# Kernel tuning notes

Hardware: AMD Instinct MI355X
Metric: run time of the kernel (lower is better)

Reference implementation:

```python
import jax, jax.numpy as jnp
import numpy as np

N_NODES = 100000
N_EDGES = 1600000
D_IN = 128
D_OUT = 128


def setup_inputs() -> dict:
    key = jax.random.key(0)
    ks = jax.random.split(key, 7)
    x = jax.random.normal(ks[0], (N_NODES, D_IN), dtype=jnp.float32)
    y = jax.random.normal(ks[1], (N_NODES, D_OUT), dtype=jnp.float32)
    edge_src = jax.random.randint(ks[2], (N_EDGES,), 0, N_NODES, dtype=jnp.int32)
    edge_dst = jax.random.randint(ks[3], (N_EDGES,), 0, N_NODES, dtype=jnp.int32)
    adj_vals = jax.random.uniform(ks[4], (N_EDGES,), dtype=jnp.float32)
    weight = jax.random.normal(ks[5], (D_IN, D_OUT), dtype=jnp.float32) * (1.0 / np.sqrt(D_IN))
    bias = jax.random.normal(ks[6], (D_OUT,), dtype=jnp.float32) * 0.01
    return {"x": x, "y": y, "edge_src": edge_src, "edge_dst": edge_dst,
            "adj_vals": adj_vals, "weight": weight, "bias": bias}


def reference(x, y, edge_src, edge_dst, adj_vals, weight, bias):
    # GraphConvolution: support = x @ W ; out = spmm(adj, support) + bias
    support = x @ weight                      # [N, d_out]
    msgs = support[edge_src] * adj_vals[:, None]   # [E, d_out] gather + scale
    agg = jax.ops.segment_sum(msgs, edge_dst, num_segments=N_NODES)  # [N, d_out]
    gc_out = agg + bias
    # ResGCN epilogue: relu(gc_out + y); dropout is identity in eval (p=0.0)
    return jax.nn.relu(gc_out + y)
```

## Files before the change

kernel.cpp:

```cpp
#include <hip/hip_runtime.h>

#define D 128
#define CE 8192
#define NB_MAX 1024
#define MAXC 512
#define EBUF 3072
#define CHUNK 1024
#define WTP 136


typedef __attribute__((ext_vector_type(8))) short bf16x8;
typedef __attribute__((ext_vector_type(4))) float f32x4;

__device__ __forceinline__ unsigned short f2bf(float f) {
  unsigned u = __float_as_uint(f);
  unsigned r = (u + 0x7fffu + ((u >> 16) & 1u)) >> 16;
  return (unsigned short)r;
}

__device__ __forceinline__ int wave_iscan(int v) {
  const int lane = threadIdx.x & 63;
#pragma unroll
  for (int off = 1; off < 64; off <<= 1) {
    int u = __shfl_up(v, off, 64);
    if (lane >= off) v += u;
  }
  return v;
}

__device__ __forceinline__ int seg_find(const int* pref, int nC, int i) {
  int lo = 0, hi = nC;
  while (hi - lo > 1) {
    int mid = (lo + hi) >> 1;
    if (pref[mid] <= i) lo = mid; else hi = mid;
  }
  return lo;
}

__global__ __launch_bounds__(256) void convert_kernel(
    const float4* __restrict__ x4, ushort4* __restrict__ xb4, int n4, int nxblk,
    const float* __restrict__ w, unsigned short* __restrict__ wt) {
  int bid = blockIdx.x;
  if (bid < nxblk) {
    int i = bid * 256 + threadIdx.x;
    if (i < n4) {
      float4 v = x4[i];
      ushort4 r;
      r.x = f2bf(v.x);
      r.y = f2bf(v.y);
      r.z = f2bf(v.z);
      r.w = f2bf(v.w);
      xb4[i] = r;
    }
  } else {
    int idx = (bid - nxblk) * 256 + threadIdx.x;
    int n = idx >> 7, k = idx & 127;
    wt[n * WTP + k] = f2bf(w[k * D + n]);
  }
}

__global__ __launch_bounds__(1024) void chunk_sort_kernel(
    const int* __restrict__ src, const int* __restrict__ dst,
    const float* __restrict__ adj, int2* __restrict__ edges,
    unsigned short* __restrict__ ofs, int nE, int nB) {
  __shared__ int2 stage[CE];
  __shared__ int h[NB_MAX + 4];
  __shared__ int wsum[16];
  const int t = threadIdx.x;
  const int c = blockIdx.x;
  const int e0 = c * CE;
  const int n = min(CE, nE - e0);
  const int lane = t & 63, wid = t >> 6;

  for (int i = t; i < NB_MAX + 4; i += 1024) h[i] = 0;
  __syncthreads();

  int dreg[8];
#pragma unroll
  for (int k = 0; k < 8; ++k) {
    int i = k * 1024 + t;
    if (i < n) {
      int d = dst[e0 + i];
      dreg[k] = d;
      atomicAdd(&h[d >> 7], 1);
    }
  }
  __syncthreads();

  int v = h[t];
  int inc = wave_iscan(v);
  if (lane == 63) wsum[wid] = inc;
  __syncthreads();
  if (wid == 0) {
    int p = (lane < 16) ? wsum[lane] : 0;
    int pi = wave_iscan(p);
    if (lane < 16) wsum[lane] = pi;
  }
  __syncthreads();
  h[t] = inc - v + (wid ? wsum[wid - 1] : 0);
  __syncthreads();

  unsigned short* o = ofs + (size_t)c * (nB + 1);
  for (int i = t; i <= nB; i += 1024)
    o[i] = (unsigned short)(i < NB_MAX ? h[i] : n);
  __syncthreads();

#pragma unroll
  for (int k = 0; k < 8; ++k) {
    int i = k * 1024 + t;
    if (i < n) {
      int d = dreg[k];
      int pos = atomicAdd(&h[d >> 7], 1);
      int2 ev;
      ev.x = src[e0 + i] | ((d & 127) << 17);
      ev.y = __float_as_int(adj[e0 + i]);
      stage[pos] = ev;
    }
  }
  __syncthreads();

  for (int i = t; i < n; i += 1024) edges[e0 + i] = stage[i];
}

__global__ __launch_bounds__(256) void bucket_fused_kernel(
    const int2* __restrict__ tmp, const unsigned short* __restrict__ ofs,
    const uint2* __restrict__ xb, const unsigned short* __restrict__ wt,
    const float* __restrict__ y, const float* __restrict__ bias,
    float* __restrict__ out, int nC, int nB, int nNodes) {
  __shared__ int2 ebuf[EBUF];
  __shared__ unsigned short agg[128 * WTP];
  __shared__ int segst[MAXC];
  __shared__ int pref[MAXC + 1];
  __shared__ int cnt[128];
  __shared__ int cur[128];
  __shared__ int sstart[128];
  __shared__ int w4[4];
  const int t = threadIdx.x;
  const int b = blockIdx.x;
  const int lane = t & 63, wid = t >> 6;

  const int c0 = 2 * t, c1 = 2 * t + 1;
  int n0 = 0, n1 = 0;
  if (c0 < nC) {
    int s0 = ofs[(size_t)c0 * (nB + 1) + b];
    int s1 = ofs[(size_t)c0 * (nB + 1) + b + 1];
    segst[c0] = c0 * CE + s0;
    n0 = s1 - s0;
  }
  if (c1 < nC) {
    int s0 = ofs[(size_t)c1 * (nB + 1) + b];
    int s1 = ofs[(size_t)c1 * (nB + 1) + b + 1];
    segst[c1] = c1 * CE + s0;
    n1 = s1 - s0;
  }
  int tt = n0 + n1;
  int inc = wave_iscan(tt);
  if (lane == 63) w4[wid] = inc;
  __syncthreads();
  int add = 0;
  for (int i = 0; i < wid; ++i) add += w4[i];
  int incl = inc + add;
  int excl = incl - tt;
  if (c0 < nC) pref[c0] = excl;
  if (c1 < nC) pref[c1] = excl + n0;
  if (t == 255) pref[nC] = incl;
  __syncthreads();
  const int m = pref[nC];

  const int gi = t >> 5;
  const int q = t & 31;
  float4 acc[16];
#pragma unroll
  for (int k = 0; k < 16; ++k) acc[k] = make_float4(0.f, 0.f, 0.f, 0.f);

  for (int w0 = 0; w0 < m; w0 += EBUF) {
    const int w1 = min(m, w0 + EBUF);
    if (t < 128) cnt[t] = 0;
    __syncthreads();

    for (int i = w0 + t; i < w1; i += 256) {
      int lo = seg_find(pref, nC, i);
      int sx = ((const int*)tmp)[(size_t)(segst[lo] + (i - pref[lo])) * 2];
      atomicAdd(&cnt[(sx >> 17) & 127], 1);
    }
    __syncthreads();

    int cv = (t < 128) ? cnt[t] : 0;
    int cinc = wave_iscan(cv);
    if (t == 63) w4[0] = cinc;
    __syncthreads();
    int cst = cinc - cv + ((t >= 64 && t < 128) ? w4[0] : 0);
    if (t < 128) {
      sstart[t] = cst;
      cur[t] = cst;
    }
    __syncthreads();

    for (int i = w0 + t; i < w1; i += 256) {
      int lo = seg_find(pref, nC, i);
      int2 ev = tmp[segst[lo] + (i - pref[lo])];
      int pos = atomicAdd(&cur[(ev.x >> 17) & 127], 1);
      ebuf[pos] = ev;
    }
    __syncthreads();

#pragma unroll
    for (int k = 0; k < 16; ++k) {
      const int dl = gi * 16 + k;
      int j = sstart[dl];
      const int e = cur[dl];
      for (; j + 3 < e; j += 4) {
        int2 e0 = ebuf[j], e1 = ebuf[j + 1], e2 = ebuf[j + 2], e3 = ebuf[j + 3];
        float a0 = __int_as_float(e0.y), a1 = __int_as_float(e1.y);
        float a2 = __int_as_float(e2.y), a3 = __int_as_float(e3.y);
        uint2 v0 = xb[(size_t)(e0.x & 0x1FFFF) * 32 + q];
        uint2 v1 = xb[(size_t)(e1.x & 0x1FFFF) * 32 + q];
        uint2 v2 = xb[(size_t)(e2.x & 0x1FFFF) * 32 + q];
        uint2 v3 = xb[(size_t)(e3.x & 0x1FFFF) * 32 + q];
        acc[k].x = fmaf(a0, __uint_as_float(v0.x << 16), acc[k].x);
        acc[k].y = fmaf(a0, __uint_as_float(v0.x & 0xffff0000u), acc[k].y);
        acc[k].z = fmaf(a0, __uint_as_float(v0.y << 16), acc[k].z);
        acc[k].w = fmaf(a0, __uint_as_float(v0.y & 0xffff0000u), acc[k].w);
        acc[k].x = fmaf(a1, __uint_as_float(v1.x << 16), acc[k].x);
        acc[k].y = fmaf(a1, __uint_as_float(v1.x & 0xffff0000u), acc[k].y);
        acc[k].z = fmaf(a1, __uint_as_float(v1.y << 16), acc[k].z);
        acc[k].w = fmaf(a1, __uint_as_float(v1.y & 0xffff0000u), acc[k].w);
        acc[k].x = fmaf(a2, __uint_as_float(v2.x << 16), acc[k].x);
        acc[k].y = fmaf(a2, __uint_as_float(v2.x & 0xffff0000u), acc[k].y);
        acc[k].z = fmaf(a2, __uint_as_float(v2.y << 16), acc[k].z);
        acc[k].w = fmaf(a2, __uint_as_float(v2.y & 0xffff0000u), acc[k].w);
        acc[k].x = fmaf(a3, __uint_as_float(v3.x << 16), acc[k].x);
        acc[k].y = fmaf(a3, __uint_as_float(v3.x & 0xffff0000u), acc[k].y);
        acc[k].z = fmaf(a3, __uint_as_float(v3.y << 16), acc[k].z);
        acc[k].w = fmaf(a3, __uint_as_float(v3.y & 0xffff0000u), acc[k].w);
      }
      for (; j < e; ++j) {
        int2 e0 = ebuf[j];
        float a0 = __int_as_float(e0.y);
        uint2 v0 = xb[(size_t)(e0.x & 0x1FFFF) * 32 + q];
        acc[k].x = fmaf(a0, __uint_as_float(v0.x << 16), acc[k].x);
        acc[k].y = fmaf(a0, __uint_as_float(v0.x & 0xffff0000u), acc[k].y);
        acc[k].z = fmaf(a0, __uint_as_float(v0.y << 16), acc[k].z);
        acc[k].w = fmaf(a0, __uint_as_float(v0.y & 0xffff0000u), acc[k].w);
      }
    }
    __syncthreads();
  }

#pragma unroll
  for (int k = 0; k < 16; ++k) {
    const int dl = gi * 16 + k;
    uint2 pk;
    pk.x = (unsigned)f2bf(acc[k].x) | ((unsigned)f2bf(acc[k].y) << 16);
    pk.y = (unsigned)f2bf(acc[k].z) | ((unsigned)f2bf(acc[k].w) << 16);
    *(uint2*)&agg[dl * WTP + q * 4] = pk;
  }
  __syncthreads();

  const int w = t >> 6, l = t & 63;
  const int quad = l >> 4, mm = l & 15;
  const int row0 = b * 128 + w * 32;
  const char* pa0 = (const char*)&agg[(w * 32 + mm) * WTP];
  const char* pa1 = (const char*)&agg[(w * 32 + 16 + mm) * WTP];

  f32x4 acc0[8], acc1[8];
#pragma unroll
  for (int nt = 0; nt < 8; ++nt) {
    acc0[nt] = (f32x4){0.f, 0.f, 0.f, 0.f};
    acc1[nt] = (f32x4){0.f, 0.f, 0.f, 0.f};
  }

#pragma unroll
  for (int ks = 0; ks < 4; ++ks) {
    const int kof = ks * 32 + quad * 8;
    bf16x8 a0 = *(const bf16x8*)(pa0 + kof * 2);
    bf16x8 a1 = *(const bf16x8*)(pa1 + kof * 2);
#pragma unroll
    for (int nt = 0; nt < 8; ++nt) {
      bf16x8 bb = *(const bf16x8*)&wt[(nt * 16 + mm) * WTP + kof];
      acc0[nt] = __builtin_amdgcn_mfma_f32_16x16x32_bf16(a0, bb, acc0[nt], 0, 0, 0);
      acc1[nt] = __builtin_amdgcn_mfma_f32_16x16x32_bf16(a1, bb, acc1[nt], 0, 0, 0);
    }
  }

  float bv[8];
#pragma unroll
  for (int nt = 0; nt < 8; ++nt) bv[nt] = bias[nt * 16 + mm];

#pragma unroll
  for (int s = 0; s < 2; ++s) {
#pragma unroll
    for (int r = 0; r < 4; ++r) {
      int row = row0 + s * 16 + quad * 4 + r;
      if (row >= nNodes) continue;
      const float* yr = y + (size_t)row * D;
      float* orow = out + (size_t)row * D;
#pragma unroll
      for (int nt = 0; nt < 8; ++nt) {
        int c = nt * 16 + mm;
        float v = (s == 0 ? acc0[nt][r] : acc1[nt][r]) + yr[c] + bv[nt];
        orow[c] = fmaxf(v, 0.f);
      }
    }
  }
}

__global__ __launch_bounds__(256) void zero_counts_kernel(int* __restrict__ c, int n) {
  int i = blockIdx.x * 256 + threadIdx.x;
  if (i < n) c[i] = 0;
}

__global__ __launch_bounds__(256) void hist_kernel(
    const int* __restrict__ dst, int* __restrict__ counts, int nE) {
  int e = blockIdx.x * 256 + threadIdx.x;
  if (e < nE) atomicAdd(&counts[dst[e]], 1);
}

__global__ __launch_bounds__(256) void scan_partial_kernel(
    const int* __restrict__ counts, int* __restrict__ chunk_sum, int n) {
  __shared__ int sdata[256];
  int b = blockIdx.x, t = threadIdx.x;
  int base = b * CHUNK + t * 4;
  int s = 0;
#pragma unroll
  for (int k = 0; k < 4; ++k) {
    int i = base + k;
    if (i < n) s += counts[i];
  }
  sdata[t] = s;
  __syncthreads();
  for (int off = 128; off > 0; off >>= 1) {
    if (t < off) sdata[t] += sdata[t + off];
    __syncthreads();
  }
  if (t == 0) chunk_sum[b] = sdata[0];
}

__global__ void scan_chunks_kernel(const int* __restrict__ chunk_sum,
                                   int* __restrict__ chunk_off,
                                   int* __restrict__ row_start, int nchunks, int n) {
  if (threadIdx.x == 0 && blockIdx.x == 0) {
    int run = 0;
    for (int i = 0; i < nchunks; ++i) {
      chunk_off[i] = run;
      run += chunk_sum[i];
    }
    row_start[n] = run;
  }
}

__global__ __launch_bounds__(256) void scan_final_kernel(
    const int* __restrict__ counts, const int* __restrict__ chunk_off,
    int* __restrict__ row_start, int* __restrict__ cursor, int n) {
  __shared__ int sdata[256];
  int b = blockIdx.x, t = threadIdx.x;
  int base = b * CHUNK + t * 4;
  int c[4] = {0, 0, 0, 0};
#pragma unroll
  for (int k = 0; k < 4; ++k) {
    int i = base + k;
    if (i < n) c[k] = counts[i];
  }
  int tsum = c[0] + c[1] + c[2] + c[3];
  sdata[t] = tsum;
  __syncthreads();
  for (int off = 1; off < 256; off <<= 1) {
    int v = (t >= off) ? sdata[t - off] : 0;
    __syncthreads();
    sdata[t] += v;
    __syncthreads();
  }
  int run = sdata[t] - tsum + chunk_off[b];
#pragma unroll
  for (int k = 0; k < 4; ++k) {
    int i = base + k;
    if (i < n) {
      row_start[i] = run;
      cursor[i] = run;
      run += c[k];
    }
  }
}

__global__ __launch_bounds__(256) void scatter_sort_kernel(
    const int* __restrict__ src, const int* __restrict__ dst,
    const float* __restrict__ adj, int* __restrict__ cursor,
    int2* __restrict__ edges, int nE) {
  int e = blockIdx.x * 256 + threadIdx.x;
  if (e >= nE) return;
  int d = dst[e];
  int2 ev;
  ev.x = src[e];
  ev.y = __float_as_int(adj[e]);
  int pos = atomicAdd(&cursor[d], 1);
  edges[pos] = ev;
}

__global__ __launch_bounds__(256) void gather_fp32_kernel(
    const float* __restrict__ x, const int* __restrict__ row_start,
    const int2* __restrict__ edges, float* __restrict__ out, int nNodes) {
  int g = (blockIdx.x * 256 + threadIdx.x) >> 5;
  int q = threadIdx.x & 31;
  if (g >= nNodes) return;
  int beg = row_start[g], end = row_start[g + 1];
  const float4* x4 = (const float4*)x;
  float4 acc = make_float4(0.f, 0.f, 0.f, 0.f);
  for (int j = beg; j < end; ++j) {
    int2 e0 = edges[j];
    float a0 = __int_as_float(e0.y);
    float4 v0 = x4[(size_t)e0.x * 32 + q];
    acc.x = fmaf(a0, v0.x, acc.x);
    acc.y = fmaf(a0, v0.y, acc.y);
    acc.z = fmaf(a0, v0.z, acc.z);
    acc.w = fmaf(a0, v0.w, acc.w);
  }
  ((float4*)out)[(size_t)g * 32 + q] = acc;
}

__global__ __launch_bounds__(256) void zero_kernel(float4* __restrict__ out, int n4) {
  int i = blockIdx.x * 256 + threadIdx.x;
  if (i < n4) out[i] = make_float4(0.f, 0.f, 0.f, 0.f);
}

__global__ __launch_bounds__(256) void scatter_atomic_kernel(
    const float* __restrict__ x, const int* __restrict__ src,
    const int* __restrict__ dst, const float* __restrict__ adj,
    float* __restrict__ out, int nE) {
  int tid = blockIdx.x * 256 + threadIdx.x;
  int e = tid >> 5;
  int q = tid & 31;
  if (e >= nE) return;
  int s = src[e];
  int d = dst[e];
  float a = adj[e];
  float4 v = ((const float4*)x)[(size_t)s * 32 + q];
  float* o = out + (size_t)d * D + q * 4;
  atomicAdd(o + 0, v.x * a);
  atomicAdd(o + 1, v.y * a);
  atomicAdd(o + 2, v.z * a);
  atomicAdd(o + 3, v.w * a);
}

__global__ __launch_bounds__(256) void gemm_fused_kernel(
    float* __restrict__ out, const float* __restrict__ w,
    const float* __restrict__ y, const float* __restrict__ bias, int nrows) {
  __shared__ float sW[D * D];
  __shared__ float sA[32 * D];
  const int tid = threadIdx.x;
  const int row0 = blockIdx.x * 32;

  const float4* w4 = (const float4*)w;
  float4* sW4 = (float4*)sW;
  for (int i = tid; i < D * D / 4; i += 256) sW4[i] = w4[i];

  const int nrow_blk = min(32, nrows - row0);
  const float4* out4_base = (const float4*)(out + (size_t)row0 * D);
  float4* sA4 = (float4*)sA;
  for (int i = tid; i < nrow_blk * 32; i += 256) sA4[i] = out4_base[i];
  __syncthreads();

  const int cg = tid & 31;
  const int rs = tid >> 5;

  float4 acc[4];
#pragma unroll
  for (int r = 0; r < 4; ++r) acc[r] = make_float4(0.f, 0.f, 0.f, 0.f);

#pragma unroll 4
  for (int k4 = 0; k4 < 32; ++k4) {
    float4 wv0 = sW4[(k4 * 4 + 0) * 32 + cg];
    float4 wv1 = sW4[(k4 * 4 + 1) * 32 + cg];
    float4 wv2 = sW4[(k4 * 4 + 2) * 32 + cg];
    float4 wv3 = sW4[(k4 * 4 + 3) * 32 + cg];
#pragma unroll
    for (int r = 0; r < 4; ++r) {
      float4 xv = sA4[(rs + r * 8) * 32 + k4];
      acc[r].x = fmaf(xv.x, wv0.x, acc[r].x);
      acc[r].y = fmaf(xv.x, wv0.y, acc[r].y);
      acc[r].z = fmaf(xv.x, wv0.z, acc[r].z);
      acc[r].w = fmaf(xv.x, wv0.w, acc[r].w);
      acc[r].x = fmaf(xv.y, wv1.x, acc[r].x);
      acc[r].y = fmaf(xv.y, wv1.y, acc[r].y);
      acc[r].z = fmaf(xv.y, wv1.z, acc[r].z);
      acc[r].w = fmaf(xv.y, wv1.w, acc[r].w);
      acc[r].x = fmaf(xv.z, wv2.x, acc[r].x);
      acc[r].y = fmaf(xv.z, wv2.y, acc[r].y);
      acc[r].z = fmaf(xv.z, wv2.z, acc[r].z);
      acc[r].w = fmaf(xv.z, wv2.w, acc[r].w);
      acc[r].x = fmaf(xv.w, wv3.x, acc[r].x);
      acc[r].y = fmaf(xv.w, wv3.y, acc[r].y);
      acc[r].z = fmaf(xv.w, wv3.z, acc[r].z);
      acc[r].w = fmaf(xv.w, wv3.w, acc[r].w);
    }
  }

  const float4* y4 = (const float4*)y;
  const float4* b4 = (const float4*)bias;
  float4* o4 = (float4*)out;
  float4 bv = b4[cg];
#pragma unroll
  for (int r = 0; r < 4; ++r) {
    int row = row0 + rs + r * 8;
    if (row < nrows) {
      float4 yv = y4[(size_t)row * 32 + cg];
      float4 res;
      res.x = fmaxf(acc[r].x + yv.x + bv.x, 0.f);
      res.y = fmaxf(acc[r].y + yv.y + bv.y, 0.f);
      res.z = fmaxf(acc[r].z + yv.z + bv.z, 0.f);
      res.w = fmaxf(acc[r].w + yv.w + bv.w, 0.f);
      o4[(size_t)row * 32 + cg] = res;
    }
  }
}

extern "C" void kernel_launch(void* const* d_in, const int* in_sizes, int n_in,
                              void* d_out, int out_size, void* d_ws, size_t ws_size,
                              hipStream_t stream) {
  const float* x    = (const float*)d_in[0];
  const float* y    = (const float*)d_in[1];
  const int*   esrc = (const int*)d_in[2];
  const int*   edst = (const int*)d_in[3];
  const float* adj  = (const float*)d_in[4];
  const float* w    = (const float*)d_in[5];
  const float* bias = (const float*)d_in[6];
  float* out = (float*)d_out;

  const int nNodes = in_sizes[0] / D;
  const int nE = in_sizes[2];
  const int n4 = nNodes * (D / 4);
  const int nB = (nNodes + 127) >> 7;
  const int nC = (nE + CE - 1) / CE;

  const size_t ofs_bytes = (((size_t)nC * (nB + 1) * 2) + 15) & ~(size_t)15;
  const size_t wt_bytes  = (size_t)D * WTP * 2;
  const size_t tmp_bytes = (size_t)nC * CE * 8;
  const size_t xb_bytes  = (size_t)nNodes * D * 2;
  const size_t need1 = ofs_bytes + wt_bytes + tmp_bytes + xb_bytes;

  const int nchunks = (nNodes + CHUNK - 1) / CHUNK;
  const size_t e2_bytes  = (size_t)nE * 8;
  const size_t int_bytes = (size_t)(3 * nNodes + 1 + 2 * nchunks) * 4;
  const size_t need2 = e2_bytes + int_bytes;

  if (ws_size >= need1 && nNodes <= NB_MAX * 128 && nC <= MAXC) {
    char* p = (char*)d_ws;
    unsigned short* ofs = (unsigned short*)p;   p += ofs_bytes;
    unsigned short* wt = (unsigned short*)p;    p += wt_bytes;
    int2* tmp = (int2*)p;                       p += tmp_bytes;
    ushort4* xb4 = (ushort4*)p;

    const int nxblk = (n4 + 255) / 256;
    chunk_sort_kernel<<<nC, 1024, 0, stream>>>(esrc, edst, adj, tmp, ofs, nE, nB);
    convert_kernel<<<nxblk + 64, 256, 0, stream>>>((const float4*)x, xb4, n4,
                                                   nxblk, w, wt);
    bucket_fused_kernel<<<nB, 256, 0, stream>>>(
        tmp, ofs, (const uint2*)xb4, wt, y, bias, out, nC, nB, nNodes);
  } else if (ws_size >= need2) {
    char* base = (char*)d_ws;
    int2* edges = (int2*)base;
    int* counts = (int*)(base + e2_bytes);
    int* row_start = counts + nNodes;
    int* cursor = row_start + nNodes + 1;
    int* chunk_sum = cursor + nNodes;
    int* chunk_off = chunk_sum + nchunks;

    zero_counts_kernel<<<(nNodes + 255) / 256, 256, 0, stream>>>(counts, nNodes);
    hist_kernel<<<(nE + 255) / 256, 256, 0, stream>>>(edst, counts, nE);
    scan_partial_kernel<<<nchunks, 256, 0, stream>>>(counts, chunk_sum, nNodes);
    scan_chunks_kernel<<<1, 64, 0, stream>>>(chunk_sum, chunk_off, row_start,
                                             nchunks, nNodes);
    scan_final_kernel<<<nchunks, 256, 0, stream>>>(counts, chunk_off, row_start,
                                                   cursor, nNodes);
    scatter_sort_kernel<<<(nE + 255) / 256, 256, 0, stream>>>(
        esrc, edst, adj, cursor, edges, nE);
    gather_fp32_kernel<<<(nNodes * 32 + 255) / 256, 256, 0, stream>>>(
        x, row_start, edges, out, nNodes);
    gemm_fused_kernel<<<(nNodes + 31) / 32, 256, 0, stream>>>(out, w, y, bias,
                                                              nNodes);
  } else {
    zero_kernel<<<(n4 + 255) / 256, 256, 0, stream>>>((float4*)out, n4);
    scatter_atomic_kernel<<<((size_t)nE * 32 + 255) / 256, 256, 0, stream>>>(
        x, esrc, edst, adj, out, nE);
    gemm_fused_kernel<<<(nNodes + 31) / 32, 256, 0, stream>>>(out, w, y, bias,
                                                              nNodes);
  }
}
```

Baseline: 310.1 us.

## Fuse chunk sort with bf16 conversion, reuse histogram ranks, alias shared memory

The chunk sort and the x/W bf16 conversion are merged into one launch, with extra blocks doing the conversion, which removes a kernel launch and lets the two phases overlap. The sort keeps the rank returned by the first histogram atomic (packed into the upper bits of the dst register), so the scatter pass needs no second atomic and one barrier is dropped. The bucket kernel overlays the agg tile on the edge buffer in one shared-memory array, with an extra barrier before agg is written, to cut LDS use and raise occupancy. Packing the rank into bits 17+ assumes node ids below 2^17 and ranks that fit in the remaining bits.

Result: faster. 299.7 us (-3.3%).

```diff
diff --git a/kernel.cpp b/kernel.cpp
--- a/kernel.cpp
+++ b/kernel.cpp
@@ -37,37 +37,42 @@
   return lo;
 }
 
-__global__ __launch_bounds__(256) void convert_kernel(
-    const float4* __restrict__ x4, ushort4* __restrict__ xb4, int n4, int nxblk,
-    const float* __restrict__ w, unsigned short* __restrict__ wt) {
-  int bid = blockIdx.x;
-  if (bid < nxblk) {
-    int i = bid * 256 + threadIdx.x;
-    if (i < n4) {
-      float4 v = x4[i];
-      ushort4 r;
-      r.x = f2bf(v.x);
-      r.y = f2bf(v.y);
-      r.z = f2bf(v.z);
-      r.w = f2bf(v.w);
-      xb4[i] = r;
-    }
-  } else {
-    int idx = (bid - nxblk) * 256 + threadIdx.x;
-    int n = idx >> 7, k = idx & 127;
-    wt[n * WTP + k] = f2bf(w[k * D + n]);
-  }
-}
-
-__global__ __launch_bounds__(1024) void chunk_sort_kernel(
+__global__ __launch_bounds__(1024) void sort_convert_kernel(
     const int* __restrict__ src, const int* __restrict__ dst,
     const float* __restrict__ adj, int2* __restrict__ edges,
-    unsigned short* __restrict__ ofs, int nE, int nB) {
+    unsigned short* __restrict__ ofs, int nE, int nB, int nC,
+    const float4* __restrict__ x4, ushort4* __restrict__ xb4, int n4,
+    int nxblk, const float* __restrict__ w, unsigned short* __restrict__ wt) {
   __shared__ int2 stage[CE];
   __shared__ int h[NB_MAX + 4];
   __shared__ int wsum[16];
+  const int bid = blockIdx.x;
   const int t = threadIdx.x;
-  const int c = blockIdx.x;
+
+  if (bid >= nC) {
+    int b2 = bid - nC;
+    if (b2 < nxblk) {
+      int i = b2 * 1024 + t;
+      if (i < n4) {
+        float4 v = x4[i];
+        ushort4 r;
+        r.x = f2bf(v.x);
+        r.y = f2bf(v.y);
+        r.z = f2bf(v.z);
+        r.w = f2bf(v.w);
+        xb4[i] = r;
+      }
+    } else {
+      int idx = (b2 - nxblk) * 1024 + t;
+      if (idx < D * D) {
+        int n = idx >> 7, k = idx & 127;
+        wt[n * WTP + k] = f2bf(w[k * D + n]);
+      }
+    }
+    return;
+  }
+
+  const int c = bid;
   const int e0 = c * CE;
   const int n = min(CE, nE - e0);
   const int lane = t & 63, wid = t >> 6;
@@ -81,8 +86,8 @@
     int i = k * 1024 + t;
     if (i < n) {
       int d = dst[e0 + i];
-      dreg[k] = d;
-      atomicAdd(&h[d >> 7], 1);
+      int rank = atomicAdd(&h[d >> 7], 1);
+      dreg[k] = d | (rank << 17);
     }
   }
   __syncthreads();
@@ -103,14 +108,15 @@
   unsigned short* o = ofs + (size_t)c * (nB + 1);
   for (int i = t; i <= nB; i += 1024)
     o[i] = (unsigned short)(i < NB_MAX ? h[i] : n);
-  __syncthreads();
 
 #pragma unroll
   for (int k = 0; k < 8; ++k) {
     int i = k * 1024 + t;
     if (i < n) {
-      int d = dreg[k];
-      int pos = atomicAdd(&h[d >> 7], 1);
+      int dr = dreg[k];
+      int d = dr & 0x1FFFF;
+      int rank = ((unsigned)dr) >> 17;
+      int pos = h[d >> 7] + rank;
       int2 ev;
       ev.x = src[e0 + i] | ((d & 127) << 17);
       ev.y = __float_as_int(adj[e0 + i]);
@@ -127,14 +133,16 @@
     const uint2* __restrict__ xb, const unsigned short* __restrict__ wt,
     const float* __restrict__ y, const float* __restrict__ bias,
     float* __restrict__ out, int nC, int nB, int nNodes) {
-  __shared__ int2 ebuf[EBUF];
-  __shared__ unsigned short agg[128 * WTP];
-  __shared__ int segst[MAXC];
-  __shared__ int pref[MAXC + 1];
-  __shared__ int cnt[128];
-  __shared__ int cur[128];
-  __shared__ int sstart[128];
-  __shared__ int w4[4];
+  __shared__ __align__(16) char smem[34816];
+  int2* ebuf  = (int2*)smem;
+  int* segst  = (int*)(smem + 24576);
+  int* pref   = (int*)(smem + 26624);
+  int* cnt    = (int*)(smem + 28680);
+  int* cur    = (int*)(smem + 29192);
+  int* sstart = (int*)(smem + 29704);
+  int* w4     = (int*)(smem + 30216);
+  unsigned short* agg = (unsigned short*)smem;
+
   const int t = threadIdx.x;
   const int b = blockIdx.x;
   const int lane = t & 63, wid = t >> 6;
@@ -246,6 +254,7 @@
     }
     __syncthreads();
   }
+  __syncthreads();
 
 #pragma unroll
   for (int k = 0; k < 16; ++k) {
@@ -549,10 +558,11 @@
     int2* tmp = (int2*)p;                       p += tmp_bytes;
     ushort4* xb4 = (ushort4*)p;
 
-    const int nxblk = (n4 + 255) / 256;
-    chunk_sort_kernel<<<nC, 1024, 0, stream>>>(esrc, edst, adj, tmp, ofs, nE, nB);
-    convert_kernel<<<nxblk + 64, 256, 0, stream>>>((const float4*)x, xb4, n4,
-                                                   nxblk, w, wt);
+    const int nxblk = (n4 + 1023) / 1024;
+    const int wtblk = (D * D + 1023) / 1024;
+    sort_convert_kernel<<<nC + nxblk + wtblk, 1024, 0, stream>>>(
+        esrc, edst, adj, tmp, ofs, nE, nB, nC,
+        (const float4*)x, xb4, n4, nxblk, w, wt);
     bucket_fused_kernel<<<nB, 256, 0, stream>>>(
         tmp, ofs, (const uint2*)xb4, wt, y, bias, out, nC, nB, nNodes);
   } else if (ws_size >= need2) {
```
